# Optimization experiments

Hardware: AMD Instinct MI355X
Metric: run time of the kernel (lower is better)

## Reference

```python
import jax, jax.numpy as jnp
import numpy as np

# __init__ defaults of BoxSelector
NMS_T = 0.5
TOP_K = 400
CONF_T = 0.5
KEEP_K = 200
# standard SSD BoxCoder variances
V0, V1 = 0.1, 0.2
BIG = 1e9
B, N, C = 128, 32768, 6  # batch, num_priors, 4 loc + 2 classes


def decode(loc, priors):
    # SSD decode: priors are (cx, cy, w, h); returns (x1, y1, x2, y2)
    cxcy = priors[:, :2] + loc[:, :2] * V0 * priors[:, 2:]
    wh = priors[:, 2:] * jnp.exp(loc[:, 2:] * V1)
    return jnp.concatenate([cxcy - wh * 0.5, cxcy + wh * 0.5], axis=1)


def pairwise_iou(b):
    # b: [K, 4] xyxy -> [K, K] IoU
    x1, y1, x2, y2 = b[:, 0], b[:, 1], b[:, 2], b[:, 3]
    area = (x2 - x1) * (y2 - y1)
    iw = jnp.clip(jnp.minimum(x2[:, None], x2[None, :]) - jnp.maximum(x1[:, None], x1[None, :]), 0.0)
    ih = jnp.clip(jnp.minimum(y2[:, None], y2[None, :]) - jnp.maximum(y1[:, None], y1[None, :]), 0.0)
    inter = iw * ih
    return inter / (area[:, None] + area[None, :] - inter + 1e-12)


def _select_image(pred, priorboxes):
    loc, confs = pred[:, :4], pred[:, 4:]
    boxes = decode(loc, priorboxes)                       # [N, 4]
    scores = jnp.max(confs, axis=1)                       # [N]
    labels = jnp.argmax(confs, axis=1)                    # [N] int
    # confidence filter (mask instead of dynamic gather, jit-friendly)
    masked = jnp.where(scores > CONF_T, scores, -BIG)
    top_s, idx = jax.lax.top_k(masked, TOP_K)             # descending, [K]
    cand_boxes = boxes[idx]                               # [K, 4]
    cand_labels = labels[idx]                             # [K]
    valid = top_s > CONF_T                                # padding from filter
    # greedy NMS over the top_k candidates (already score-sorted desc)
    iou = pairwise_iou(cand_boxes)                        # [K, K]
    j = jnp.arange(TOP_K)
    def body(i, keep):
        sup = keep[i] & (iou[i] > NMS_T) & (j > i)
        return keep & ~sup
    keep = jax.lax.fori_loop(0, TOP_K, body, valid)
    # original sorts kept scores ASCENDING and takes the first keep_top_k
    sort_key = jnp.where(keep, top_s, BIG)                # invalid sort last
    order = jnp.argsort(sort_key)[:KEEP_K]                # [keep_top_k]
    out = jnp.concatenate(
        [cand_labels[order, None].astype(jnp.float32),
         top_s[order, None],
         cand_boxes[order]], axis=1)                      # [keep_top_k, 6]
    return jnp.where(keep[order][:, None], out, 0.0)


def setup_inputs() -> dict:
    key = jax.random.key(0)
    k1, k2 = jax.random.split(key)
    predictions = jax.random.normal(k1, (B, N, C), dtype=jnp.float32)
    priors = jax.random.uniform(k2, (N, 4), dtype=jnp.float32)
    return {"predictions": predictions, "priors": priors}


def reference(predictions, priors):
    priorboxes = priors[:, :4]
    return jax.vmap(lambda p: _select_image(p, priorboxes))(predictions)  # [B, keep_top_k, 6]
```

## Files before the change

### kernel.cpp

```cpp
#include <hip/hip_runtime.h>
#include <stdint.h>

#define BB 128
#define NN 32768
#define CI 6
#define TOPK 400
#define PADK 448
#define KEEPK 200
#define SORTN 1024
#define NT 1024
#define KQT 8
#define NBUCK 4096
#define KEY0 0x3F000000u
#define STILE 1024

#define IOU_C 0.50000002980232238769531250

__global__ __launch_bounds__(256) void score_kernel(
        const float* __restrict__ pred, uint32_t* __restrict__ keys) {
    __shared__ float lf[STILE * 6];
    const int t = threadIdx.x;
    const float4* p4 = reinterpret_cast<const float4*>(pred) +
                       (size_t)blockIdx.x * (STILE * 6 / 4);
    float4* l4 = reinterpret_cast<float4*>(lf);
#pragma unroll
    for (int k = 0; k < 6; k++) l4[t + 256 * k] = p4[t + 256 * k];
    __syncthreads();
    uint4 o;
    { float s = fmaxf(lf[24 * t +  4], lf[24 * t +  5]); o.x = (s > 0.5f) ? __float_as_uint(s) : 0u; }
    { float s = fmaxf(lf[24 * t + 10], lf[24 * t + 11]); o.y = (s > 0.5f) ? __float_as_uint(s) : 0u; }
    { float s = fmaxf(lf[24 * t + 16], lf[24 * t + 17]); o.z = (s > 0.5f) ? __float_as_uint(s) : 0u; }
    { float s = fmaxf(lf[24 * t + 22], lf[24 * t + 23]); o.w = (s > 0.5f) ? __float_as_uint(s) : 0u; }
    reinterpret_cast<uint4*>(keys)[blockIdx.x * 256 + t] = o;
}

__global__ __launch_bounds__(NT) void boxsel2_kernel(
        const float* __restrict__ pred, const float* __restrict__ priors,
        const uint32_t* __restrict__ keys, float* __restrict__ out) {
    const int b = blockIdx.x;
    const int tid = threadIdx.x;
    const int lane = tid & 63;
    const int wid = tid >> 6;
    const float* img = pred + (size_t)b * (NN * CI);
    float* oimg = out + (size_t)b * KEEPK * 6;

    __shared__ union {
        unsigned int hist[4][NBUCK];
        struct {
            unsigned long long cbuf[SORTN];
            float4 cbox[PADK];
            float car[PADK], csc[TOPK];
            int clab[TOPK];
            unsigned long long supm[TOPK * 7 + 8];
        } s;
    } u;
    __shared__ unsigned int wavetot[16];
    __shared__ unsigned int sh_bucket, ccount;
    __shared__ unsigned long long keepw[8];

    for (int i = tid; i < KEEPK * 6; i += NT) oimg[i] = 0.0f;

    uint4 kq[KQT];
    const uint4* k4 = reinterpret_cast<const uint4*>(keys + (size_t)b * NN);
#pragma unroll
    for (int uu = 0; uu < KQT; uu++) kq[uu] = k4[tid + (uu << 10)];

    if (tid == 0) { sh_bucket = 0; ccount = 0; }
    for (int i = tid; i < 4 * NBUCK; i += NT) ((unsigned int*)u.hist)[i] = 0u;
    __syncthreads();

    const int hc = wid & 3;
#pragma unroll
    for (int uu = 0; uu < KQT; uu++) {
        uint32_t k0 = kq[uu].x, k1 = kq[uu].y, k2 = kq[uu].z, k3 = kq[uu].w;
        if (k0) { unsigned int bu = (k0 - KEY0) >> 13; if (bu > NBUCK - 1u) bu = NBUCK - 1u; atomicAdd(&u.hist[hc][bu], 1u); }
        if (k1) { unsigned int bu = (k1 - KEY0) >> 13; if (bu > NBUCK - 1u) bu = NBUCK - 1u; atomicAdd(&u.hist[hc][bu], 1u); }
        if (k2) { unsigned int bu = (k2 - KEY0) >> 13; if (bu > NBUCK - 1u) bu = NBUCK - 1u; atomicAdd(&u.hist[hc][bu], 1u); }
        if (k3) { unsigned int bu = (k3 - KEY0) >> 13; if (bu > NBUCK - 1u) bu = NBUCK - 1u; atomicAdd(&u.hist[hc][bu], 1u); }
    }
    __syncthreads();

    unsigned int h0 = u.hist[0][4 * tid + 0] + u.hist[1][4 * tid + 0] + u.hist[2][4 * tid + 0] + u.hist[3][4 * tid + 0];
    unsigned int h1 = u.hist[0][4 * tid + 1] + u.hist[1][4 * tid + 1] + u.hist[2][4 * tid + 1] + u.hist[3][4 * tid + 1];
    unsigned int h2 = u.hist[0][4 * tid + 2] + u.hist[1][4 * tid + 2] + u.hist[2][4 * tid + 2] + u.hist[3][4 * tid + 2];
    unsigned int h3 = u.hist[0][4 * tid + 3] + u.hist[1][4 * tid + 3] + u.hist[2][4 * tid + 3] + u.hist[3][4 * tid + 3];
    unsigned int sum = h0 + h1 + h2 + h3;
    unsigned int suf = sum;
#pragma unroll
    for (int off = 1; off < 64; off <<= 1) {
        unsigned int v = __shfl_down(suf, off);
        if (lane + off < 64) suf += v;
    }
    if (lane == 0) wavetot[wid] = suf;
    __syncthreads();
    if (tid < 16) {
        unsigned int wv = wavetot[tid];
        unsigned int ws = wv;
#pragma unroll
        for (int off = 1; off < 16; off <<= 1) {
            unsigned int v = __shfl_down(ws, off);
            if (tid + off < 16) ws += v;
        }
        wavetot[tid] = ws - wv;
    }
    __syncthreads();
    unsigned int acc = wavetot[wid] + (suf - sum);
    if (acc < TOPK && acc + h3 >= TOPK) sh_bucket = 4 * tid + 3;
    acc += h3;
    if (acc < TOPK && acc + h2 >= TOPK) sh_bucket = 4 * tid + 2;
    acc += h2;
    if (acc < TOPK && acc + h1 >= TOPK) sh_bucket = 4 * tid + 1;
    acc += h1;
    if (acc < TOPK && acc + h0 >= TOPK) sh_bucket = 4 * tid + 0;
    __syncthreads();
    const uint32_t Tkey = KEY0 + (sh_bucket << 13);

#pragma unroll
    for (int uu = 0; uu < KQT; uu++) {
        uint32_t kk[4] = { kq[uu].x, kq[uu].y, kq[uu].z, kq[uu].w };
#pragma unroll
        for (int j = 0; j < 4; j++) {
            uint32_t key = kk[j];
            if (key >= Tkey) {
                unsigned int p = atomicAdd(&ccount, 1u);
                if (p < SORTN) {
                    unsigned int idx = ((unsigned int)(tid + (uu << 10)) << 2) + (unsigned int)j;
                    u.s.cbuf[p] = ((unsigned long long)key << 32) |
                                  (unsigned long long)(0xFFFFFFFFu - idx);
                }
            }
        }
    }
    __syncthreads();

    const unsigned int cnt = (ccount < SORTN) ? ccount : SORTN;
    for (int i2 = tid; i2 < TOPK * 7 + 8; i2 += NT) u.s.supm[i2] = 0ull;
    if (tid >= TOPK && tid < PADK) {
        u.s.cbox[tid] = make_float4(0.f, 0.f, 0.f, 0.f);
        u.s.car[tid] = 0.f;
    }
    if (tid < 8) {
        int cntc = (cnt < TOPK) ? (int)cnt : TOPK;
        int rem = cntc - (tid << 6);
        keepw[tid] = (rem <= 0) ? 0ull : ((rem >= 64) ? ~0ull : ((1ull << rem) - 1ull));
    }
    if ((unsigned int)tid < cnt) {
        unsigned long long ct = u.s.cbuf[tid];
        uint32_t key = (uint32_t)(ct >> 32);
        uint32_t idx = 0xFFFFFFFFu - (uint32_t)(ct & 0xFFFFFFFFull);
        const float* p = img + (size_t)idx * CI;
        float l0 = p[0], l1 = p[1], l2 = p[2], l3 = p[3], c0 = p[4], c1 = p[5];
        const float* pr = priors + (size_t)idx * 4;
        float px = pr[0], py = pr[1], pw = pr[2], ph = pr[3];
        unsigned int rank = 0;
        const ulonglong2* c2 = reinterpret_cast<const ulonglong2*>(u.s.cbuf);
        unsigned int half = cnt >> 1;
#pragma unroll 4
        for (unsigned int m = 0; m < half; m++) {
            ulonglong2 v = c2[m];
            rank += (v.x > ct) ? 1u : 0u;
            rank += (v.y > ct) ? 1u : 0u;
        }
        if (cnt & 1) rank += (u.s.cbuf[cnt - 1] > ct) ? 1u : 0u;
        float cxv = __fadd_rn(px, __fmul_rn(__fmul_rn(l0, 0.1f), pw));
        float cyv = __fadd_rn(py, __fmul_rn(__fmul_rn(l1, 0.1f), ph));
        float ew = __fmul_rn(pw, expf(__fmul_rn(l2, 0.2f)));
        float eh = __fmul_rn(ph, expf(__fmul_rn(l3, 0.2f)));
        float hw = __fmul_rn(ew, 0.5f);
        float hh = __fmul_rn(eh, 0.5f);
        float x1 = __fsub_rn(cxv, hw), y1 = __fsub_rn(cyv, hh);
        float x2 = __fadd_rn(cxv, hw), y2 = __fadd_rn(cyv, hh);
        if (rank < TOPK) {
            u.s.cbox[rank] = make_float4(x1, y1, x2, y2);
            u.s.car[rank] = __fmul_rn(__fsub_rn(x2, x1), __fsub_rn(y2, y1));
            u.s.csc[rank] = __uint_as_float(key);
            u.s.clab[rank] = (c1 > c0) ? 1 : 0;
        }
    }
    __syncthreads();

    {
        float4 bjv[7]; float ajv[7];
#pragma unroll
        for (int jw = 0; jw < 7; jw++) {
            int j = (jw << 6) + lane;
            bjv[jw] = u.s.cbox[j];
            ajv[jw] = u.s.car[j];
        }
        float4 bi = u.s.cbox[wid];
        float ai = u.s.car[wid];
        for (int i = wid; i < TOPK; i += 16) {
            float4 bi_n = u.s.cbox[i + 16];
            float ai_n = u.s.car[i + 16];
            const int jw0 = i >> 6;
            unsigned long long dmask = (~0ull << (i & 63)) << 1;
#pragma unroll
            for (int jw = 0; jw < 7; jw++) {
                if (jw < jw0) continue;
                float4 bj = bjv[jw]; float aj = ajv[jw];
                float iw = fmaxf(__fsub_rn(fminf(bi.z, bj.z), fmaxf(bi.x, bj.x)), 0.0f);
                float ih = fmaxf(__fsub_rn(fminf(bi.w, bj.w), fmaxf(bi.y, bj.y)), 0.0f);
                float inter = __fmul_rn(iw, ih);
                float denom = __fadd_rn(__fsub_rn(__fadd_rn(ai, aj), inter), 1e-12f);
                bool bit = (double)inter > (double)denom * IOU_C;
                unsigned long long word = __ballot(bit);
                if (lane == 0) {
                    if (jw == jw0) word &= dmask;
                    u.s.supm[i * 7 + jw] = word;
                }
            }
            bi = bi_n; ai = ai_n;
        }
    }
    __syncthreads();

    if (tid < 64) {
        int w = tid & 7;
        unsigned long long kw = keepw[w];
        unsigned long long rr[16], nn[16];
#pragma unroll
        for (int k = 0; k < 16; k++) rr[k] = u.s.supm[k * 7 + w];
        for (int base = 0; base < TOPK; base += 16) {
            int nb = base + 16;
            int gb = (nb < TOPK) ? nb : base;
#pragma unroll
            for (int k = 0; k < 16; k++) nn[k] = u.s.supm[(gb + k) * 7 + w];
#pragma unroll
            for (int k = 0; k < 16; k++) {
                int i = base + k;
                unsigned int lo = (unsigned int)__builtin_amdgcn_readlane((int)(unsigned int)kw, i >> 6);
                unsigned int hi = (unsigned int)__builtin_amdgcn_readlane((int)(unsigned int)(kw >> 32), i >> 6);
                unsigned int sel = ((i & 63) < 32) ? lo : hi;
                if ((sel >> (i & 31)) & 1u) kw &= ~rr[k];
            }
#pragma unroll
            for (int k = 0; k < 16; k++) rr[k] = nn[k];
        }
        if (tid < 7) keepw[tid] = kw;
    }
    __syncthreads();

    if (tid < TOPK) {
        const int t = tid;
        if ((keepw[t >> 6] >> (t & 63)) & 1ull) {
            float st = u.s.csc[t];
            int rank = 0;
#pragma unroll
            for (int w = 0; w < 7; w++) {
                unsigned long long kws = keepw[w];
                int jb = w << 6;
                unsigned long long m;
                if (t >= jb + 63)      m = 0ull;
                else if (t < jb)       m = ~0ull;
                else                   m = ~((1ull << (t - jb + 1)) - 1ull);
                rank += __popcll(kws & m);
            }
            for (int j = t + 1; j < TOPK && u.s.csc[j] == st; j++)
                if ((keepw[j >> 6] >> (j & 63)) & 1ull) rank--;
            for (int j = t - 1; j >= 0 && u.s.csc[j] == st; j--)
                if ((keepw[j >> 6] >> (j & 63)) & 1ull) rank++;
            if (rank < KEEPK) {
                float4 bx = u.s.cbox[t];
                float* row = oimg + (size_t)rank * 6;
                row[0] = (float)u.s.clab[t];
                row[1] = st;
                row[2] = bx.x; row[3] = bx.y; row[4] = bx.z; row[5] = bx.w;
            }
        }
    }
}

extern "C" void kernel_launch(void* const* d_in, const int* in_sizes, int n_in,
                              void* d_out, int out_size, void* d_ws, size_t ws_size,
                              hipStream_t stream) {
    const float* pred = (const float*)d_in[0];
    const float* priors = (const float*)d_in[1];
    float* out = (float*)d_out;
    uint32_t* keys = (uint32_t*)d_ws;
    score_kernel<<<(BB * NN) / STILE, 256, 0, stream>>>(pred, keys);
    boxsel2_kernel<<<BB, NT, 0, stream>>>(pred, priors, keys, out);
}
```

Before: 196.9 us.

## Use wave-aggregated atomics for compaction and readlane-based rank counting

```diff
diff --git a/kernel.cpp b/kernel.cpp
--- a/kernel.cpp
+++ b/kernel.cpp
@@ -66,7 +66,11 @@
     for (int uu = 0; uu < KQT; uu++) kq[uu] = k4[tid + (uu << 10)];
 
     if (tid == 0) { sh_bucket = 0; ccount = 0; }
-    for (int i = tid; i < 4 * NBUCK; i += NT) ((unsigned int*)u.hist)[i] = 0u;
+    {
+        uint4* hz = reinterpret_cast<uint4*>(u.hist);
+#pragma unroll
+        for (int k = 0; k < 4; k++) hz[tid + k * NT] = make_uint4(0u, 0u, 0u, 0u);
+    }
     __syncthreads();
 
     const int hc = wid & 3;
@@ -121,12 +125,21 @@
 #pragma unroll
         for (int j = 0; j < 4; j++) {
             uint32_t key = kk[j];
-            if (key >= Tkey) {
-                unsigned int p = atomicAdd(&ccount, 1u);
-                if (p < SORTN) {
-                    unsigned int idx = ((unsigned int)(tid + (uu << 10)) << 2) + (unsigned int)j;
-                    u.s.cbuf[p] = ((unsigned long long)key << 32) |
-                                  (unsigned long long)(0xFFFFFFFFu - idx);
+            bool pr = (key >= Tkey);
+            unsigned long long m = __ballot(pr);
+            if (m != 0ull) {
+                int leader = (int)(__ffsll((long long)m) - 1);
+                unsigned int base = 0;
+                if (lane == leader) base = atomicAdd(&ccount, (unsigned int)__popcll(m));
+                base = (unsigned int)__shfl((int)base, leader);
+                if (pr) {
+                    unsigned int pfx = (unsigned int)__popcll(m & ((1ull << lane) - 1ull));
+                    unsigned int p = base + pfx;
+                    if (p < SORTN) {
+                        unsigned int idx = ((unsigned int)(tid + (uu << 10)) << 2) + (unsigned int)j;
+                        u.s.cbuf[p] = ((unsigned long long)key << 32) |
+                                      (unsigned long long)(0xFFFFFFFFu - idx);
+                    }
                 }
             }
         }
@@ -143,6 +156,16 @@
         int cntc = (cnt < TOPK) ? (int)cnt : TOPK;
         int rem = cntc - (tid << 6);
         keepw[tid] = (rem <= 0) ? 0ull : ((rem >= 64) ? ~0ull : ((1ull << rem) - 1ull));
+    }
+    unsigned long long rv0 = 0, rv1 = 0, rv2 = 0, rv3 = 0, rv4 = 0, rv5 = 0, rv6 = 0;
+    if ((unsigned int)(wid << 6) < cnt) {
+        rv0 = u.s.cbuf[lane];
+        rv1 = u.s.cbuf[64 + lane];
+        rv2 = u.s.cbuf[128 + lane];
+        rv3 = u.s.cbuf[192 + lane];
+        rv4 = u.s.cbuf[256 + lane];
+        rv5 = u.s.cbuf[320 + lane];
+        rv6 = u.s.cbuf[384 + lane];
     }
     if ((unsigned int)tid < cnt) {
         unsigned long long ct = u.s.cbuf[tid];
@@ -153,15 +176,24 @@
         const float* pr = priors + (size_t)idx * 4;
         float px = pr[0], py = pr[1], pw = pr[2], ph = pr[3];
         unsigned int rank = 0;
-        const ulonglong2* c2 = reinterpret_cast<const ulonglong2*>(u.s.cbuf);
-        unsigned int half = cnt >> 1;
-#pragma unroll 4
-        for (unsigned int m = 0; m < half; m++) {
-            ulonglong2 v = c2[m];
-            rank += (v.x > ct) ? 1u : 0u;
-            rank += (v.y > ct) ? 1u : 0u;
-        }
-        if (cnt & 1) rank += (u.s.cbuf[cnt - 1] > ct) ? 1u : 0u;
+#define RCHUNK(K, RV)                                                         \
+        { unsigned int basej = (unsigned int)(K) << 6;                        \
+          if (basej < cnt) {                                                  \
+            unsigned int lim = cnt - basej; if (lim > 64u) lim = 64u;         \
+            for (unsigned int j2 = 0; j2 < lim; j2++) {                       \
+                unsigned int blo = (unsigned int)__builtin_amdgcn_readlane(   \
+                    (int)(unsigned int)(RV), (int)j2);                        \
+                unsigned int bhi = (unsigned int)__builtin_amdgcn_readlane(   \
+                    (int)(unsigned int)((RV) >> 32), (int)j2);                \
+                unsigned long long bj =                                       \
+                    ((unsigned long long)bhi << 32) | (unsigned long long)blo;\
+                rank += (bj > ct) ? 1u : 0u;                                  \
+            } } }
+        RCHUNK(0, rv0) RCHUNK(1, rv1) RCHUNK(2, rv2) RCHUNK(3, rv3)
+        RCHUNK(4, rv4) RCHUNK(5, rv5) RCHUNK(6, rv6)
+#undef RCHUNK
+        for (unsigned int jj = 448; jj < cnt; jj++)
+            rank += (u.s.cbuf[jj] > ct) ? 1u : 0u;
         float cxv = __fadd_rn(px, __fmul_rn(__fmul_rn(l0, 0.1f), pw));
         float cyv = __fadd_rn(py, __fmul_rn(__fmul_rn(l1, 0.1f), ph));
         float ew = __fmul_rn(pw, expf(__fmul_rn(l2, 0.2f)));
```

New measurement: 207.8 us. 1.06x slower.

## Replace full rank-count sort with bucket-ordered scatter and intra-bucket ranking

Applied to the files above, without the earlier changes.

```diff
diff --git a/kernel.cpp b/kernel.cpp
--- a/kernel.cpp
+++ b/kernel.cpp
@@ -54,8 +54,10 @@
             unsigned long long supm[TOPK * 7 + 8];
         } s;
     } u;
+    __shared__ __align__(16) unsigned int hsuf[NBUCK];
+    __shared__ __align__(16) unsigned int bcnt[NBUCK];
     __shared__ unsigned int wavetot[16];
-    __shared__ unsigned int sh_bucket, ccount;
+    __shared__ unsigned int sh_bucket, sh_cnt;
     __shared__ unsigned long long keepw[8];
 
     for (int i = tid; i < KEEPK * 6; i += NT) oimg[i] = 0.0f;
@@ -65,8 +67,13 @@
 #pragma unroll
     for (int uu = 0; uu < KQT; uu++) kq[uu] = k4[tid + (uu << 10)];
 
-    if (tid == 0) { sh_bucket = 0; ccount = 0; }
-    for (int i = tid; i < 4 * NBUCK; i += NT) ((unsigned int*)u.hist)[i] = 0u;
+    if (tid == 0) { sh_bucket = 0; sh_cnt = 0; }
+    {
+        uint4* hz = reinterpret_cast<uint4*>(u.hist);
+#pragma unroll
+        for (int k = 0; k < 4; k++) hz[tid + k * NT] = make_uint4(0u, 0u, 0u, 0u);
+        reinterpret_cast<uint4*>(bcnt)[tid] = make_uint4(0u, 0u, 0u, 0u);
+    }
     __syncthreads();
 
     const int hc = wid & 3;
@@ -93,6 +100,7 @@
     }
     if (lane == 0) wavetot[wid] = suf;
     __syncthreads();
+    u.s.cbuf[tid] = 0ull;
     if (tid < 16) {
         unsigned int wv = wavetot[tid];
         unsigned int ws = wv;
@@ -104,16 +112,23 @@
         wavetot[tid] = ws - wv;
     }
     __syncthreads();
-    unsigned int acc = wavetot[wid] + (suf - sum);
-    if (acc < TOPK && acc + h3 >= TOPK) sh_bucket = 4 * tid + 3;
-    acc += h3;
-    if (acc < TOPK && acc + h2 >= TOPK) sh_bucket = 4 * tid + 2;
-    acc += h2;
-    if (acc < TOPK && acc + h1 >= TOPK) sh_bucket = 4 * tid + 1;
-    acc += h1;
-    if (acc < TOPK && acc + h0 >= TOPK) sh_bucket = 4 * tid + 0;
+    {
+        unsigned int a3 = wavetot[wid] + (suf - sum);
+        unsigned int a2 = a3 + h3;
+        unsigned int a1 = a2 + h2;
+        unsigned int a0 = a1 + h1;
+        unsigned int tot = a0 + h0;
+        *reinterpret_cast<uint4*>(&hsuf[4 * tid]) = make_uint4(a0, a1, a2, a3);
+        if (a3 < TOPK && a2 >= TOPK)  { sh_bucket = 4 * tid + 3; sh_cnt = a2; }
+        if (a2 < TOPK && a1 >= TOPK)  { sh_bucket = 4 * tid + 2; sh_cnt = a1; }
+        if (a1 < TOPK && a0 >= TOPK)  { sh_bucket = 4 * tid + 1; sh_cnt = a0; }
+        if (a0 < TOPK && tot >= TOPK) { sh_bucket = 4 * tid + 0; sh_cnt = tot; }
+        if (tid == 0 && tot < TOPK) sh_cnt = tot;
+    }
     __syncthreads();
     const uint32_t Tkey = KEY0 + (sh_bucket << 13);
+    const unsigned int cnt = sh_cnt;
+    const unsigned int cntS = (cnt < SORTN) ? cnt : SORTN;
 
 #pragma unroll
     for (int uu = 0; uu < KQT; uu++) {
@@ -122,18 +137,41 @@
         for (int j = 0; j < 4; j++) {
             uint32_t key = kk[j];
             if (key >= Tkey) {
-                unsigned int p = atomicAdd(&ccount, 1u);
-                if (p < SORTN) {
+                unsigned int bu = (key - KEY0) >> 13;
+                if (bu > NBUCK - 1u) bu = NBUCK - 1u;
+                unsigned int prov = hsuf[bu] + atomicAdd(&bcnt[bu], 1u);
+                if (prov < SORTN) {
                     unsigned int idx = ((unsigned int)(tid + (uu << 10)) << 2) + (unsigned int)j;
-                    u.s.cbuf[p] = ((unsigned long long)key << 32) |
-                                  (unsigned long long)(0xFFFFFFFFu - idx);
+                    u.s.cbuf[prov] = ((unsigned long long)key << 32) |
+                                     (unsigned long long)(0xFFFFFFFFu - idx);
                 }
             }
         }
     }
     __syncthreads();
 
-    const unsigned int cnt = (ccount < SORTN) ? ccount : SORTN;
+    {
+        unsigned long long ct = 0ull; unsigned int rk = 0; bool act = false;
+        if ((unsigned int)tid < cntS) {
+            ct = u.s.cbuf[tid];
+            uint32_t key = (uint32_t)(ct >> 32);
+            unsigned int bu = (key - KEY0) >> 13;
+            if (bu > NBUCK - 1u) bu = NBUCK - 1u;
+            unsigned int gs = hsuf[bu], gc = bcnt[bu];
+            rk = (unsigned int)tid;
+            if (gc > 1u) {
+                unsigned int ge = gs + gc; if (ge > SORTN) ge = SORTN;
+                rk = gs;
+                for (unsigned int k = gs; k < ge; k++)
+                    rk += (u.s.cbuf[k] > ct) ? 1u : 0u;
+                act = (rk != (unsigned int)tid);
+            }
+        }
+        __syncthreads();
+        if (act && rk < SORTN) u.s.cbuf[rk] = ct;
+    }
+    __syncthreads();
+
     for (int i2 = tid; i2 < TOPK * 7 + 8; i2 += NT) u.s.supm[i2] = 0ull;
     if (tid >= TOPK && tid < PADK) {
         u.s.cbox[tid] = make_float4(0.f, 0.f, 0.f, 0.f);
@@ -144,38 +182,33 @@
         int rem = cntc - (tid << 6);
         keepw[tid] = (rem <= 0) ? 0ull : ((rem >= 64) ? ~0ull : ((1ull << rem) - 1ull));
     }
-    if ((unsigned int)tid < cnt) {
-        unsigned long long ct = u.s.cbuf[tid];
-        uint32_t key = (uint32_t)(ct >> 32);
-        uint32_t idx = 0xFFFFFFFFu - (uint32_t)(ct & 0xFFFFFFFFull);
-        const float* p = img + (size_t)idx * CI;
-        float l0 = p[0], l1 = p[1], l2 = p[2], l3 = p[3], c0 = p[4], c1 = p[5];
-        const float* pr = priors + (size_t)idx * 4;
-        float px = pr[0], py = pr[1], pw = pr[2], ph = pr[3];
-        unsigned int rank = 0;
-        const ulonglong2* c2 = reinterpret_cast<const ulonglong2*>(u.s.cbuf);
-        unsigned int half = cnt >> 1;
-#pragma unroll 4
-        for (unsigned int m = 0; m < half; m++) {
-            ulonglong2 v = c2[m];
-            rank += (v.x > ct) ? 1u : 0u;
-            rank += (v.y > ct) ? 1u : 0u;
-        }
-        if (cnt & 1) rank += (u.s.cbuf[cnt - 1] > ct) ? 1u : 0u;
-        float cxv = __fadd_rn(px, __fmul_rn(__fmul_rn(l0, 0.1f), pw));
-        float cyv = __fadd_rn(py, __fmul_rn(__fmul_rn(l1, 0.1f), ph));
-        float ew = __fmul_rn(pw, expf(__fmul_rn(l2, 0.2f)));
-        float eh = __fmul_rn(ph, expf(__fmul_rn(l3, 0.2f)));
-        float hw = __fmul_rn(ew, 0.5f);
-        float hh = __fmul_rn(eh, 0.5f);
-        float x1 = __fsub_rn(cxv, hw), y1 = __fsub_rn(cyv, hh);
-        float x2 = __fadd_rn(cxv, hw), y2 = __fadd_rn(cyv, hh);
-        if (rank < TOPK) {
-            u.s.cbox[rank] = make_float4(x1, y1, x2, y2);
-            u.s.car[rank] = __fmul_rn(__fsub_rn(x2, x1), __fsub_rn(y2, y1));
-            u.s.csc[rank] = __uint_as_float(key);
-            u.s.clab[rank] = (c1 > c0) ? 1 : 0;
-        }
+    if (tid < TOPK) {
+        const int t = tid;
+        unsigned long long c = u.s.cbuf[t];
+        uint32_t key = (uint32_t)(c >> 32);
+        uint32_t idx = 0xFFFFFFFFu - (uint32_t)(c & 0xFFFFFFFFull);
+        int valid = (key != 0u) && (idx < NN);
+        float x1 = 0.f, y1 = 0.f, x2 = 0.f, y2 = 0.f;
+        int lab = 0;
+        if (valid) {
+            const float* p = img + (size_t)idx * CI;
+            float l0 = p[0], l1 = p[1], l2 = p[2], l3 = p[3], c0 = p[4], c1 = p[5];
+            const float* pr = priors + (size_t)idx * 4;
+            float px = pr[0], py = pr[1], pw = pr[2], ph = pr[3];
+            float cxv = __fadd_rn(px, __fmul_rn(__fmul_rn(l0, 0.1f), pw));
+            float cyv = __fadd_rn(py, __fmul_rn(__fmul_rn(l1, 0.1f), ph));
+            float ew = __fmul_rn(pw, expf(__fmul_rn(l2, 0.2f)));
+            float eh = __fmul_rn(ph, expf(__fmul_rn(l3, 0.2f)));
+            float hw = __fmul_rn(ew, 0.5f);
+            float hh = __fmul_rn(eh, 0.5f);
+            x1 = __fsub_rn(cxv, hw); y1 = __fsub_rn(cyv, hh);
+            x2 = __fadd_rn(cxv, hw); y2 = __fadd_rn(cyv, hh);
+            lab = (c1 > c0) ? 1 : 0;
+        }
+        u.s.cbox[t] = make_float4(x1, y1, x2, y2);
+        u.s.csc[t] = __uint_as_float(key);
+        u.s.car[t] = __fmul_rn(__fsub_rn(x2, x1), __fsub_rn(y2, y1));
+        u.s.clab[t] = lab;
     }
     __syncthreads();
 
```

Result: no change. 194.1 us (-1.4%).
